# Kernel optimization log

Measured on AMD Instinct MI355X. Metric: run time of the kernel, lower is better.

Reference implementation:

```python
import jax, jax.numpy as jnp
import numpy as np

IN_SIZE, HID_SIZE, OUT_SIZE = 256, 512, 256
BATCH, NSTEPS = 64, 2048


def setup_inputs() -> dict:
    key = jax.random.key(0)
    ks = jax.random.split(key, 6)
    s_ih = 1.0 / np.sqrt(IN_SIZE)
    s_hh = 1.0 / np.sqrt(HID_SIZE)
    return {
        "input": jax.random.normal(ks[0], (BATCH, NSTEPS, IN_SIZE), dtype=jnp.float32),
        "w_ih": jax.random.uniform(ks[1], (HID_SIZE, IN_SIZE), jnp.float32, -s_ih, s_ih),
        "w_hh": jax.random.uniform(ks[2], (HID_SIZE, HID_SIZE), jnp.float32, -s_hh, s_hh),
        "b_h": jax.random.uniform(ks[3], (HID_SIZE,), jnp.float32, -s_hh, s_hh),
        "w_out": jax.random.uniform(ks[4], (OUT_SIZE, HID_SIZE), jnp.float32, -s_hh, s_hh),
        "b_out": jax.random.uniform(ks[5], (OUT_SIZE,), jnp.float32, -s_hh, s_hh),
    }


def reference(input, w_ih, w_hh, b_h, w_out, b_out):
    # Vanilla RNN recurrence (delay=1 in the original forward) + linear readout.
    # h_t = tanh(x_t W_ih^T + h_{t-1} W_hh^T + b_h);  y_t = h_t W_out^T + b_out
    batch = input.shape[0]
    h0 = jnp.zeros((batch, w_hh.shape[0]), dtype=input.dtype)
    # Precompute input projections for all steps in one big GEMM (same math).
    x_proj = jnp.einsum("bti,hi->bth", input, w_ih) + b_h  # [B, T, H]

    def step(h, xp_t):
        h_new = jnp.tanh(xp_t + h @ w_hh.T)
        return h_new, h_new

    _, hs = jax.lax.scan(step, h0, jnp.swapaxes(x_proj, 0, 1))  # hs: [T, B, H]
    hs = jnp.swapaxes(hs, 0, 1)  # [B, T, H]
    outputs = jnp.einsum("bth,oh->bto", hs, w_out) + b_out  # [B, T, O]
    return outputs
```

## Files before the change

kernel.cpp:

```cpp
#include <hip/hip_runtime.h>


typedef _Float16 f16;
typedef __attribute__((ext_vector_type(2))) _Float16 half2_t;
typedef __attribute__((ext_vector_type(4))) float float4_t;

#define NIN    256
#define NHID   512
#define NOUT   256
#define NBATCH 64
#define NT     2048

#define FL4(p) (*reinterpret_cast<const float4_t*>(p))
#define LOADA(p)     __hip_atomic_load((p), __ATOMIC_RELAXED, __HIP_MEMORY_SCOPE_AGENT)
#define STOREA(p, v) __hip_atomic_store((p), (v), __ATOMIC_RELAXED, __HIP_MEMORY_SCOPE_AGENT)

#define LDS_BAR() do {                                              \
    asm volatile("s_waitcnt lgkmcnt(0)\n\ts_barrier" ::: "memory"); \
    __builtin_amdgcn_sched_barrier(0);                              \
  } while (0)

#if __has_builtin(__builtin_amdgcn_fdot2)
__device__ __forceinline__ float fdot2f(half2_t a, half2_t b, float c) {
  return __builtin_amdgcn_fdot2(a, b, c, false);
}
#else
__device__ __forceinline__ float fdot2f(half2_t a, half2_t b, float c) {
  return c + (float)a.x * (float)b.x + (float)a.y * (float)b.y;
}
#endif

__device__ __forceinline__ float tanh_fast(float x) {
  float e = __expf(2.0f * x);
  return 1.0f - 2.0f / (e + 1.0f);
}

__device__ unsigned long long g_pub[NBATCH][2][NHID];

__global__ __launch_bounds__(256) void k_zero() {
  ((unsigned long long*)g_pub)[blockIdx.x * 256 + threadIdx.x] = 0ull;
}

__global__ __launch_bounds__(256) void k_inproj(
    const float* __restrict__ x, const float* __restrict__ w,
    const float* __restrict__ bias, float* __restrict__ xplo, float* __restrict__ xphi)
{
  __shared__ float xs[32][260];
  __shared__ float wsT[8][520];
  const int t = threadIdx.x;
  const int m0 = blockIdx.x * 32;
  const int mthr = t & 3;
  const int nthr = t >> 2;

  #pragma unroll
  for (int r = 0; r < 8; ++r) {
    int f = (t + 256 * r) * 4;
    int row = f >> 8, col = f & 255;
    *(float4_t*)&xs[row][col] =
        *reinterpret_cast<const float4_t*>(x + (size_t)(m0 + row) * NIN + col);
  }

  float acc[8][8];
  #pragma unroll
  for (int nn = 0; nn < 8; ++nn) {
    float bv = bias[nthr * 8 + nn];
    #pragma unroll
    for (int mm = 0; mm < 8; ++mm) acc[nn][mm] = bv;
  }

  for (int kc = 0; kc < 32; ++kc) {
    __syncthreads();
    #pragma unroll
    for (int r = 0; r < 4; ++r) {
      int f = (t + 256 * r) * 4;
      int n = f >> 3, k0 = f & 7;
      float4_t v = *reinterpret_cast<const float4_t*>(w + (size_t)n * NIN + kc * 8 + k0);
      #pragma unroll
      for (int j = 0; j < 4; ++j) wsT[k0 + j][n] = v[j];
    }
    __syncthreads();
    #pragma unroll
    for (int kp = 0; kp < 8; ++kp) {
      float4_t wv0 = *(const float4_t*)&wsT[kp][nthr * 8];
      float4_t wv1 = *(const float4_t*)&wsT[kp][nthr * 8 + 4];
      #pragma unroll
      for (int mm = 0; mm < 8; ++mm) {
        float xv = xs[mthr * 8 + mm][kc * 8 + kp];
        acc[0][mm] = fmaf(wv0.x, xv, acc[0][mm]);
        acc[1][mm] = fmaf(wv0.y, xv, acc[1][mm]);
        acc[2][mm] = fmaf(wv0.z, xv, acc[2][mm]);
        acc[3][mm] = fmaf(wv0.w, xv, acc[3][mm]);
        acc[4][mm] = fmaf(wv1.x, xv, acc[4][mm]);
        acc[5][mm] = fmaf(wv1.y, xv, acc[5][mm]);
        acc[6][mm] = fmaf(wv1.z, xv, acc[6][mm]);
        acc[7][mm] = fmaf(wv1.w, xv, acc[7][mm]);
      }
    }
  }

  const int n0 = nthr * 8;
  float* dst = (n0 < 256) ? (xplo + n0) : (xphi + (n0 - 256));
  #pragma unroll
  for (int mm = 0; mm < 8; ++mm) {
    int m = m0 + mthr * 8 + mm;
    float4_t o0 = {acc[0][mm], acc[1][mm], acc[2][mm], acc[3][mm]};
    float4_t o1 = {acc[4][mm], acc[5][mm], acc[6][mm], acc[7][mm]};
    *reinterpret_cast<float4_t*>(dst + (size_t)m * 256)     = o0;
    *reinterpret_cast<float4_t*>(dst + (size_t)m * 256 + 4) = o1;
  }
}

__global__ __launch_bounds__(512, 1) void k_recur(
    const float* __restrict__ whh, float* outbuf, float* wsbuf)
{
  __shared__ __align__(16) float hb[2][NHID];
  __shared__ __align__(16) float pacc[8][128];
  const int g = blockIdx.x;
  const int b = (g >> 5) * 8 + (g & 7);
  const int q = (g >> 3) & 3;
  const int t = threadIdx.x;
  const int js = t & 63;
  const int ks = t >> 6;
  const int r0 = q * 128 + js * 2, r1 = r0 + 1;
  const bool ownk = (ks >> 1) == q;
  const int prow = (q * 128 + 128 + t) & 511;

  float4_t w0[16], w1[16];
  #pragma unroll
  for (int i = 0; i < 16; ++i) {
    w0[i] = FL4(whh + (size_t)r0 * NHID + ks * 64 + i * 4);
    w1[i] = FL4(whh + (size_t)r1 * NHID + ks * 64 + i * 4);
  }

  float* xp = ((q < 2) ? (outbuf + q * 128) : (wsbuf + (q - 2) * 128))
              + (size_t)b * NT * 256 + t;
  float xq0 = 0.f, xq1 = 0.f;
  if (t < 128) { xq0 = xp[0]; xq1 = xp[256]; }

  hb[0][t] = 0.0f;
  __syncthreads();

  for (int s = 0; s < NT; ++s) {
    float* hbc = hb[s & 1];
    float* hbn = hb[(s & 1) ^ 1];

    const bool rd = (s > 0) && (t < 384);
    unsigned long long pv = 0;
    if (rd) pv = LOADA(&g_pub[b][(s - 1) & 1][prow]);

    float4_t a0 = {0.f,0.f,0.f,0.f}, a1 = {0.f,0.f,0.f,0.f};
    float4_t b0 = {0.f,0.f,0.f,0.f}, b1 = {0.f,0.f,0.f,0.f};
    if (ownk) {
      const float4_t* h4 = (const float4_t*)&hbc[ks * 64];
      #pragma unroll
      for (int i = 0; i < 16; i += 2) {
        float4_t hA = h4[i], hB = h4[i + 1];
        a0 += w0[i] * hA;  a1 += w0[i + 1] * hB;
        b0 += w1[i] * hA;  b1 += w1[i + 1] * hB;
      }
    }

    if (rd) {
      while ((unsigned)(pv >> 32) < (unsigned)s)
        pv = LOADA(&g_pub[b][(s - 1) & 1][prow]);
      hbc[prow] = __builtin_bit_cast(float, (unsigned)pv);
    }
    LDS_BAR();

    if (!ownk) {
      const float4_t* h4 = (const float4_t*)&hbc[ks * 64];
      #pragma unroll
      for (int i = 0; i < 16; i += 2) {
        float4_t hA = h4[i], hB = h4[i + 1];
        a0 += w0[i] * hA;  a1 += w0[i + 1] * hB;
        b0 += w1[i] * hA;  b1 += w1[i + 1] * hB;
      }
    }

    float4_t av = a0 + a1, bv = b0 + b1;
    pacc[ks][js * 2]     = (av.x + av.y) + (av.z + av.w);
    pacc[ks][js * 2 + 1] = (bv.x + bv.y) + (bv.z + bv.w);
    LDS_BAR();

    if (t < 128) {
      float sum = pacc[0][t];
      #pragma unroll
      for (int k2 = 1; k2 < 8; ++k2) sum += pacc[k2][t];
      float h = tanh_fast(sum + xq0);
      STOREA(&g_pub[b][s & 1][q * 128 + t],
             ((unsigned long long)(unsigned)(s + 1) << 32) |
             (unsigned long long)__builtin_bit_cast(unsigned, h));
      hbn[q * 128 + t] = h;
      xp[(size_t)s * 256] = h;
      xq0 = xq1;
      if (s + 2 < NT) xq1 = xp[(size_t)(s + 2) * 256];
    }
    LDS_BAR();
  }
}

__global__ __launch_bounds__(256) void k_outproj(
    const float* hlo, const float* hhi, const float* __restrict__ w,
    const float* __restrict__ bias, float* out)
{
  __shared__ half2_t xs[32][258];
  __shared__ half2_t ws[256][19];
  const int t = threadIdx.x;
  const int m0 = blockIdx.x * 32;
  const int nthr = t >> 2;
  const int mthr = t & 3;

  #pragma unroll
  for (int r = 0; r < 16; ++r) {
    int f = (t + 256 * r) * 4;
    int row = f >> 9, col = f & 511;
    const float* src = (col < 256) ? (hlo + (size_t)(m0 + row) * 256 + col)
                                   : (hhi + (size_t)(m0 + row) * 256 + (col - 256));
    float4_t v = *reinterpret_cast<const float4_t*>(src);
    xs[row][(col >> 1)]     = half2_t{(f16)v.x, (f16)v.y};
    xs[row][(col >> 1) + 1] = half2_t{(f16)v.z, (f16)v.w};
  }

  float acc[4][8];
  #pragma unroll
  for (int nn = 0; nn < 4; ++nn) {
    float bv = bias[nthr * 4 + nn];
    #pragma unroll
    for (int mm = 0; mm < 8; ++mm) acc[nn][mm] = bv;
  }

  for (int kc = 0; kc < 16; ++kc) {
    __syncthreads();
    #pragma unroll
    for (int r = 0; r < 8; ++r) {
      int f = (t + 256 * r) * 4;
      int row = f >> 5, col = f & 31;
      float4_t v = *reinterpret_cast<const float4_t*>(w + (size_t)row * NHID + kc * 32 + col);
      ws[row][(col >> 1)]     = half2_t{(f16)v.x, (f16)v.y};
      ws[row][(col >> 1) + 1] = half2_t{(f16)v.z, (f16)v.w};
    }
    __syncthreads();
    #pragma unroll
    for (int kp = 0; kp < 16; ++kp) {
      half2_t wv[4], xv[8];
      #pragma unroll
      for (int nn = 0; nn < 4; ++nn) wv[nn] = ws[nthr * 4 + nn][kp];
      #pragma unroll
      for (int mm = 0; mm < 8; ++mm) xv[mm] = xs[mthr * 8 + mm][kc * 16 + kp];
      #pragma unroll
      for (int nn = 0; nn < 4; ++nn)
        #pragma unroll
        for (int mm = 0; mm < 8; ++mm)
          acc[nn][mm] = fdot2f(wv[nn], xv[mm], acc[nn][mm]);
    }
  }

  #pragma unroll
  for (int mm = 0; mm < 8; ++mm) {
    int m = m0 + mthr * 8 + mm;
    float4_t o = {acc[0][mm], acc[1][mm], acc[2][mm], acc[3][mm]};
    *reinterpret_cast<float4_t*>(out + (size_t)m * NOUT + nthr * 4) = o;
  }
}

extern "C" void kernel_launch(void* const* d_in, const int* in_sizes, int n_in,
                              void* d_out, int out_size, void* d_ws, size_t ws_size,
                              hipStream_t stream) {
  (void)in_sizes; (void)n_in; (void)ws_size; (void)out_size;
  const float* x     = (const float*)d_in[0];
  const float* w_ih  = (const float*)d_in[1];
  const float* w_hh  = (const float*)d_in[2];
  const float* b_h   = (const float*)d_in[3];
  const float* w_out = (const float*)d_in[4];
  const float* b_out = (const float*)d_in[5];

  float* outb = (float*)d_out;
  float* wsb  = (float*)d_ws;

  k_zero   <<<256, 256, 0, stream>>>();
  k_inproj <<<(NBATCH * NT) / 32, 256, 0, stream>>>(x, w_ih, b_h, outb, wsb);
  k_recur  <<<256, 512, 0, stream>>>(w_hh, outb, wsb);
  k_outproj<<<(NBATCH * NT) / 32, 256, 0, stream>>>(outb, wsb, w_out, b_out, outb);
}
```

Baseline: 3.740 ms.

## Restructure recurrence step so each wave polls its own h slice, one barrier

Each thread now polls the published hidden value whose index equals its own thread id and writes it to LDS. Every wave then reads only the 64-element h segment it wrote itself, so the full dot product can start without a block-wide barrier. The partial-sum buffer is double-buffered by step parity, which removes the trailing barrier, cutting three barriers per step to one. In exchange, the owned-slice compute no longer overlaps the cross-block polling, and correctness relies on the wave-local matching between poll index and read segment.

Result: slower. 4.256 ms (+13.8%).

```diff
diff --git a/kernel.cpp b/kernel.cpp
--- a/kernel.cpp
+++ b/kernel.cpp
@@ -113,8 +113,8 @@
 __global__ __launch_bounds__(512, 1) void k_recur(
     const float* __restrict__ whh, float* outbuf, float* wsbuf)
 {
-  __shared__ __align__(16) float hb[2][NHID];
-  __shared__ __align__(16) float pacc[8][128];
+  __shared__ __align__(16) float hl[2][NHID];
+  __shared__ __align__(16) float pacc[2][8][128];
   const int g = blockIdx.x;
   const int b = (g >> 5) * 8 + (g & 7);
   const int q = (g >> 3) & 3;
@@ -122,8 +122,7 @@
   const int js = t & 63;
   const int ks = t >> 6;
   const int r0 = q * 128 + js * 2, r1 = r0 + 1;
-  const bool ownk = (ks >> 1) == q;
-  const int prow = (q * 128 + 128 + t) & 511;
+  const bool ownw = (ks >> 1) == q;
 
   float4_t w0[16], w1[16];
   #pragma unroll
@@ -132,26 +131,29 @@
     w1[i] = FL4(whh + (size_t)r1 * NHID + ks * 64 + i * 4);
   }
 
-  float* xp = ((q < 2) ? (outbuf + q * 128) : (wsbuf + (q - 2) * 128))
-              + (size_t)b * NT * 256 + t;
+  float* xp = ((t < 256) ? (outbuf + t) : (wsbuf + (t - 256))) + (size_t)b * NT * 256;
   float xq0 = 0.f, xq1 = 0.f;
-  if (t < 128) { xq0 = xp[0]; xq1 = xp[256]; }
-
-  hb[0][t] = 0.0f;
+  if (ownw) { xq0 = xp[0]; xq1 = xp[256]; }
+
+  hl[0][t] = 0.0f;
   __syncthreads();
 
   for (int s = 0; s < NT; ++s) {
-    float* hbc = hb[s & 1];
-    float* hbn = hb[(s & 1) ^ 1];
-
-    const bool rd = (s > 0) && (t < 384);
-    unsigned long long pv = 0;
-    if (rd) pv = LOADA(&g_pub[b][(s - 1) & 1][prow]);
+    const int par = s & 1;
+
+    if (!ownw && s > 0) {
+      unsigned long long pv = LOADA(&g_pub[b][(s - 1) & 1][t]);
+      while ((unsigned)(pv >> 32) < (unsigned)s)
+        pv = LOADA(&g_pub[b][(s - 1) & 1][t]);
+      hl[par][t] = __builtin_bit_cast(float, (unsigned)pv);
+      asm volatile("s_waitcnt lgkmcnt(0)" ::: "memory");
+      __builtin_amdgcn_sched_barrier(0);
+    }
 
     float4_t a0 = {0.f,0.f,0.f,0.f}, a1 = {0.f,0.f,0.f,0.f};
     float4_t b0 = {0.f,0.f,0.f,0.f}, b1 = {0.f,0.f,0.f,0.f};
-    if (ownk) {
-      const float4_t* h4 = (const float4_t*)&hbc[ks * 64];
+    {
+      const float4_t* h4 = (const float4_t*)&hl[par][ks * 64];
       #pragma unroll
       for (int i = 0; i < 16; i += 2) {
         float4_t hA = h4[i], hB = h4[i + 1];
@@ -159,43 +161,26 @@
         b0 += w1[i] * hA;  b1 += w1[i + 1] * hB;
       }
     }
-
-    if (rd) {
-      while ((unsigned)(pv >> 32) < (unsigned)s)
-        pv = LOADA(&g_pub[b][(s - 1) & 1][prow]);
-      hbc[prow] = __builtin_bit_cast(float, (unsigned)pv);
-    }
+    float4_t av = a0 + a1, bv = b0 + b1;
+    pacc[par][ks][js * 2]     = (av.x + av.y) + (av.z + av.w);
+    pacc[par][ks][js * 2 + 1] = (bv.x + bv.y) + (bv.z + bv.w);
     LDS_BAR();
 
-    if (!ownk) {
-      const float4_t* h4 = (const float4_t*)&hbc[ks * 64];
-      #pragma unroll
-      for (int i = 0; i < 16; i += 2) {
-        float4_t hA = h4[i], hB = h4[i + 1];
-        a0 += w0[i] * hA;  a1 += w0[i + 1] * hB;
-        b0 += w1[i] * hA;  b1 += w1[i + 1] * hB;
-      }
-    }
-
-    float4_t av = a0 + a1, bv = b0 + b1;
-    pacc[ks][js * 2]     = (av.x + av.y) + (av.z + av.w);
-    pacc[ks][js * 2 + 1] = (bv.x + bv.y) + (bv.z + bv.w);
-    LDS_BAR();
-
-    if (t < 128) {
-      float sum = pacc[0][t];
-      #pragma unroll
-      for (int k2 = 1; k2 < 8; ++k2) sum += pacc[k2][t];
+    if (ownw) {
+      const int lr = t & 127;
+      float sum = ((pacc[par][0][lr] + pacc[par][1][lr]) +
+                   (pacc[par][2][lr] + pacc[par][3][lr])) +
+                  ((pacc[par][4][lr] + pacc[par][5][lr]) +
+                   (pacc[par][6][lr] + pacc[par][7][lr]));
       float h = tanh_fast(sum + xq0);
-      STOREA(&g_pub[b][s & 1][q * 128 + t],
+      STOREA(&g_pub[b][par][t],
              ((unsigned long long)(unsigned)(s + 1) << 32) |
              (unsigned long long)__builtin_bit_cast(unsigned, h));
-      hbn[q * 128 + t] = h;
+      hl[par ^ 1][t] = h;
       xp[(size_t)s * 256] = h;
       xq0 = xq1;
       if (s + 2 < NT) xq1 = xp[(size_t)(s + 2) * 256];
     }
-    LDS_BAR();
   }
 }
 
```
